# Kernel tuning notes

Measured on AMD Instinct MI355X. Metric: run time of the kernel, lower is better.

The kernel has to match this reference:

```python
import jax, jax.numpy as jnp
import numpy as np

N_TOKEN = 392
POS_WEIGHT = 1.0
LOSS_WEIGHT = 1.0


def _cam_map(logits, w_proj, xf, shape):
    # logits: (B, K_cls); w_proj: (K_cls, C); xf: (B, C, N)
    B, T, H, W = shape
    top_cls = jnp.argmax(logits, axis=1)                 # sort desc -> [0] == argmax
    w_top = w_proj[top_cls]                              # (B, C) gather top-class weight row
    row = jnp.einsum('bc,bcn->bn', w_top, xf)            # (B, N) per-sample CAM scores
    mn = row.min(axis=1, keepdims=True)
    mx = row.max(axis=1, keepdims=True)
    rown = (row - mn) / (mx - mn)                        # min-max normalize
    vals, idxs = jax.lax.top_k(rown, N_TOKEN)            # (B, 392)
    hw = H * W
    ti = idxs // hw
    hi = (idxs % hw) // W
    wi = idxs % W
    bi = jnp.broadcast_to(jnp.arange(B)[:, None], idxs.shape)
    cam = jnp.zeros((B, T, H, W), rown.dtype).at[bi, ti, hi, wi].set(vals)
    return cam


def _forward(x, pred_v_logits, pred_n_logits, w_proj_v, w_proj_n,
             conv_w, conv_b, score_w, score_b):
    B, C, T, H, W = x.shape
    xf = x.reshape(B, C, T * H * W)
    cam_v = _cam_map(pred_v_logits, w_proj_v, xf, (B, T, H, W))
    cam_n = _cam_map(pred_n_logits, w_proj_n, xf, (B, T, H, W))
    cam_gt = jnp.maximum(cam_v, cam_n)                   # torch.where(v > n, v, n)
    cam_gt = jax.lax.stop_gradient(cam_gt)               # original builds it from numpy + .detach()

    dn = ('NCDHW', 'OIDHW', 'NCDHW')
    h1 = jax.nn.relu(
        jax.lax.conv_general_dilated(x, conv_w, (1, 1, 1),
                                     [(0, 0), (1, 1), (1, 1)],
                                     dimension_numbers=dn)
        + conv_b[None, :, None, None, None])
    logits = (jax.lax.conv_general_dilated(h1, score_w, (1, 1, 1),
                                           [(0, 0), (0, 0), (0, 0)],
                                           dimension_numbers=dn)
              + score_b[None, :, None, None, None])      # (B,1,T,H,W)

    xcam = logits[:, 0].reshape(B * T, H * W)
    y = cam_gt.reshape(B * T, H * W)
    # BCEWithLogitsLoss(pos_weight) mean
    bce = -(POS_WEIGHT * y * jax.nn.log_sigmoid(xcam)
            + (1.0 - y) * jax.nn.log_sigmoid(-xcam))
    return LOSS_WEIGHT * bce.mean()


def setup_inputs() -> dict:
    key = jax.random.key(0)
    ks = jax.random.split(key, 8)
    B, C, T, H, W = 64, 256, 32, 7, 7
    Kv, Kn, D = 97, 300, 512
    x = jax.random.normal(ks[0], (B, C, T, H, W), jnp.float32)
    pred_v_logits = jax.random.normal(ks[1], (B, Kv), jnp.float32)
    pred_n_logits = jax.random.normal(ks[2], (B, Kn), jnp.float32)
    w_proj_v = jax.random.normal(ks[3], (Kv, C), jnp.float32) / np.sqrt(C)
    w_proj_n = jax.random.normal(ks[4], (Kn, C), jnp.float32) / np.sqrt(C)
    conv_w = jax.random.normal(ks[5], (D, C, 1, 3, 3), jnp.float32) / np.sqrt(C * 9)
    conv_b = jnp.zeros((D,), jnp.float32)
    score_w = jax.random.normal(ks[6], (1, D, 1, 1, 1), jnp.float32) / np.sqrt(D)
    score_b = jnp.zeros((1,), jnp.float32)
    return {"x": x, "pred_v_logits": pred_v_logits, "pred_n_logits": pred_n_logits,
            "w_proj_v": w_proj_v, "w_proj_n": w_proj_n,
            "conv_w": conv_w, "conv_b": conv_b,
            "score_w": score_w, "score_b": score_b}


def reference(x, pred_v_logits, pred_n_logits, w_proj_v, w_proj_n,
              conv_w, conv_b, score_w, score_b):
    return _forward(x, pred_v_logits, pred_n_logits, w_proj_v, w_proj_n,
                    conv_w, conv_b, score_w, score_b)
```

## Files before the change

kernel.cpp:

```cpp
#include <hip/hip_runtime.h>
#include <hip/hip_bf16.h>
#include <math.h>

#define BB 64
#define CC 256
#define TT 32
#define HH 7
#define WW 7
#define HW 49
#define NN 1568
#define KV 97
#define KN 300
#define DD 512
#define NTOK 392
#define TOTAL (BB*TT*HW)
#define BCAP 256
#define XP_P 257

typedef float f32x4 __attribute__((ext_vector_type(4)));
typedef short bf16x8 __attribute__((ext_vector_type(8)));

#define GLDS(g, l) __builtin_amdgcn_global_load_lds(                          \
    (const __attribute__((address_space(1))) void*)(g),                       \
    (__attribute__((address_space(3))) void*)(l), 16, 0, 0)

__global__ __launch_bounds__(256) void k_xp(
        const float* __restrict__ x, __hip_bfloat16* __restrict__ xp,
        const float* __restrict__ pv, const float* __restrict__ pn,
        const float* __restrict__ wpv, const float* __restrict__ wpn,
        const float* __restrict__ cw, __hip_bfloat16* __restrict__ wb,
        float* __restrict__ rowv, float* __restrict__ rown_,
        int* __restrict__ counter) {
    __shared__ float xs2[HW * XP_P + 7];
    __shared__ float wvs[CC], wns[CC];
    __shared__ float psum[4 * HW];
    __shared__ int cls_sh[2];
    int bt = blockIdx.x;
    int tid = threadIdx.x;
    int b = bt >> 5, t = bt & 31;
    int lane = tid & 63;
    if (bt == 0 && tid == 0) *counter = 0;

    {
        int base = bt * 576;
        #pragma unroll
        for (int r = 0; r < 3; ++r) {
            int o = base + r * 256 + tid;
            if (o < base + 576) {
                int kk = o / (DD * CC);
                int rem = o - kk * (DD * CC);
                int d = rem >> 8, c = rem & 255;
                wb[o] = __float2bfloat16(cw[(d * CC + c) * 9 + kk]);
            }
        }
    }

    if (tid < 128) {
        int head = tid >> 6;
        const float* r = head ? (pn + b * KN) : (pv + b * KV);
        int K = head ? KN : KV;
        float best = -1e30f; int bi = 0x7fffffff;
        for (int k = lane; k < K; k += 64) {
            float v = r[k];
            if (v > best || (v == best && k < bi)) { best = v; bi = k; }
        }
        #pragma unroll
        for (int off = 32; off >= 1; off >>= 1) {
            float ov = __shfl_xor(best, off);
            int oi = __shfl_xor(bi, off);
            if (ov > best || (ov == best && oi < bi)) { best = ov; bi = oi; }
        }
        if (lane == 0) cls_sh[head] = bi;
    }

    const float* xb = x + ((size_t)b * CC * TT + t) * HW;
    for (int i = tid; i < CC * HW; i += 256) {
        int c = i / HW, q = i - (i / HW) * HW;
        xs2[q * XP_P + c] = xb[(size_t)c * (TT * HW) + q];
    }
    __syncthreads();
    wvs[tid] = wpv[cls_sh[0] * CC + tid];
    wns[tid] = wpn[cls_sh[1] * CC + tid];
    __syncthreads();

    __hip_bfloat16* xpb = xp + (size_t)bt * 81 * CC;
    for (int u = tid; u < 81 * 32; u += 256) {
        int p = u >> 5, c0 = (u & 31) * 8;
        int hh = p / 9, ww = p - (p / 9) * 9;
        bool inb = (hh >= 1 && hh <= 7 && ww >= 1 && ww <= 7);
        const float* row = xs2 + ((hh - 1) * 7 + (ww - 1)) * XP_P + c0;
        bf16x8 pack;
        #pragma unroll
        for (int j = 0; j < 8; ++j) {
            float v = inb ? row[j] : 0.f;
            __hip_bfloat16 bv = __float2bfloat16(v);
            pack[j] = *reinterpret_cast<short*>(&bv);
        }
        *reinterpret_cast<bf16x8*>(xpb + p * 256 + c0) = pack;
    }

    if (tid < 4 * HW) {
        int sel = tid / HW;
        int q = tid - sel * HW;
        const float* w = (sel < 2) ? wvs : wns;
        int cb2 = (sel & 1) * 128;
        const float* row = xs2 + q * XP_P + cb2;
        float s = 0.f;
        #pragma unroll 4
        for (int c = 0; c < 128; ++c) s = fmaf(w[cb2 + c], row[c], s);
        psum[tid] = s;
    }
    __syncthreads();
    if (tid < 2 * HW) {
        int head = tid >= HW;
        int q = head ? tid - HW : tid;
        float s = head ? (psum[2 * HW + q] + psum[3 * HW + q])
                       : (psum[q] + psum[HW + q]);
        (head ? rown_ : rowv)[bt * HW + q] = s;
    }
}

__device__ __forceinline__ int binof(float v) {
    int i = (int)(v * 1024.f);
    return i < 0 ? 0 : (i > 1023 ? 1023 : i);
}

__device__ void cam_block(int b, int tid, char* smem,
                          const float* __restrict__ rowv,
                          const float* __restrict__ rown_,
                          float* __restrict__ cam) {
    float* rv = (float*)smem;
    float* rn = (float*)(smem + 6272);
    int* h = (int*)(smem + 12544);
    int* tsum = (int*)(smem + 16640);
    float* lval_v = (float*)(smem + 17664);
    int* lidx_v = (int*)(smem + 18688);
    float* lval_n = (float*)(smem + 19712);
    int* lidx_n = (int*)(smem + 20736);
    float* wred = (float*)(smem + 21760);
    int* sc = (int*)(smem + 21824);

    for (int n = tid; n < NN; n += 256) { rv[n] = rowv[b * NN + n]; rn[n] = rown_[b * NN + n]; }
    __syncthreads();
    float mnv = 1e30f, mxv = -1e30f, mnn = 1e30f, mxn = -1e30f;
    for (int n = tid; n < NN; n += 256) {
        float v = rv[n]; mnv = fminf(mnv, v); mxv = fmaxf(mxv, v);
        float u = rn[n]; mnn = fminf(mnn, u); mxn = fmaxf(mxn, u);
    }
    #pragma unroll
    for (int off = 32; off >= 1; off >>= 1) {
        mnv = fminf(mnv, __shfl_xor(mnv, off));
        mxv = fmaxf(mxv, __shfl_xor(mxv, off));
        mnn = fminf(mnn, __shfl_xor(mnn, off));
        mxn = fmaxf(mxn, __shfl_xor(mxn, off));
    }
    if ((tid & 63) == 0) {
        int wid = tid >> 6;
        wred[wid * 4 + 0] = mnv; wred[wid * 4 + 1] = mxv;
        wred[wid * 4 + 2] = mnn; wred[wid * 4 + 3] = mxn;
    }
    if (tid == 0) { sc[0] = 0; sc[1] = 0; }
    __syncthreads();
    mnv = fminf(fminf(wred[0], wred[4]), fminf(wred[8], wred[12]));
    mxv = fmaxf(fmaxf(wred[1], wred[5]), fmaxf(wred[9], wred[13]));
    mnn = fminf(fminf(wred[2], wred[6]), fminf(wred[10], wred[14]));
    mxn = fmaxf(fmaxf(wred[3], wred[7]), fmaxf(wred[11], wred[15]));
    float iv = 1.f / (mxv - mnv), inn = 1.f / (mxn - mnn);

    for (int n = tid; n < NN; n += 256) {
        rv[n] = (rv[n] - mnv) * iv;
        rn[n] = (rn[n] - mnn) * inn;
    }
    for (int i = tid; i < 1024; i += 256) h[i] = 0;
    __syncthreads();
    for (int n = tid; n < NN; n += 256) {
        atomicAdd(&h[binof(rv[n])], 1);
        atomicAdd(&h[binof(rn[n])], 1 << 16);
    }
    __syncthreads();

    int h0 = h[4 * tid], h1 = h[4 * tid + 1], h2 = h[4 * tid + 2], h3 = h[4 * tid + 3];
    tsum[tid] = h0 + h1 + h2 + h3;
    __syncthreads();
    for (int off = 1; off < 256; off <<= 1) {
        int add = (tid + off < 256) ? tsum[tid + off] : 0;
        __syncthreads();
        tsum[tid] += add;
        __syncthreads();
    }
    {
        int scur = tsum[tid];
        int hk[4] = {h0, h1, h2, h3};
        #pragma unroll
        for (int k = 0; k < 4; ++k) {
            int snext = scur - hk[k];
            int scv = scur & 0xffff, ncv = snext & 0xffff;
            int sh = scur >> 16, nh = snext >> 16;
            if (scv >= NTOK && ncv < NTOK) { sc[2] = 4 * tid + k; sc[3] = ncv; }
            if (sh >= NTOK && nh < NTOK) { sc[4] = 4 * tid + k; sc[5] = nh; }
            scur = snext;
        }
    }
    __syncthreads();
    int bsv = sc[2], abv = sc[3], bsn = sc[4], abn = sc[5];

    for (int n = tid; n < NN; n += 256) {
        float v = rv[n]; int bv = binof(v);
        if (bv < bsv) rv[n] = 0.f;
        else if (bv == bsv) {
            int s = atomicAdd(&sc[0], 1);
            if (s < BCAP) { lval_v[s] = v; lidx_v[s] = n; }
        }
        float u = rn[n]; int bu = binof(u);
        if (bu < bsn) rn[n] = 0.f;
        else if (bu == bsn) {
            int s = atomicAdd(&sc[1], 1);
            if (s < BCAP) { lval_n[s] = u; lidx_n[s] = n; }
        }
    }
    __syncthreads();
    int Lv = sc[0] < BCAP ? sc[0] : BCAP;
    int Ln = sc[1] < BCAP ? sc[1] : BCAP;
    for (int i = tid; i < Lv; i += 256) {
        float vi = lval_v[i]; int ni = lidx_v[i]; int r = 0;
        for (int j = 0; j < Lv; ++j) {
            float vj = lval_v[j]; int nj = lidx_v[j];
            r += (vj > vi || (vj == vi && nj < ni)) ? 1 : 0;
        }
        rv[ni] = (r < NTOK - abv) ? vi : 0.f;
    }
    for (int i = tid; i < Ln; i += 256) {
        float vi = lval_n[i]; int ni = lidx_n[i]; int r = 0;
        for (int j = 0; j < Ln; ++j) {
            float vj = lval_n[j]; int nj = lidx_n[j];
            r += (vj > vi || (vj == vi && nj < ni)) ? 1 : 0;
        }
        rn[ni] = (r < NTOK - abn) ? vi : 0.f;
    }
    __syncthreads();
    for (int n = tid; n < NN; n += 256) cam[b * NN + n] = fmaxf(rv[n], rn[n]);
}

__global__ __launch_bounds__(256, 3) void k_gemm(
        const __hip_bfloat16* __restrict__ xp, const __hip_bfloat16* __restrict__ wb,
        const float* __restrict__ convb, const float* __restrict__ scorew,
        float* __restrict__ pl, const float* __restrict__ rowv,
        const float* __restrict__ rown_, float* __restrict__ cam) {
    __shared__ char smem[32768];
    int tid = threadIdx.x;
    int bid = blockIdx.x;
    if (bid < 64) { cam_block(bid, tid, smem, rowv, rown_, cam); return; }
    char* As = smem;
    char* Bs = smem + 16384;
    int gid = bid - 64;
    int xcd = gid & 7;
    int local = gid >> 3;
    int mtile = xcd * 98 + (local >> 2);
    int nblk = local & 3;
    int m0 = mtile * 128;
    int n0 = nblk * 128;
    int lane = tid & 63, wv = tid >> 6;
    int wm = wv >> 1, wn = wv & 1;
    int ln = lane & 15, qd = lane >> 4;

    int rrow = tid >> 3;
    int segst = ((tid & 7) ^ (rrow & 7)) * 8;
    int bt_[4], hh_[4], ww_[4];
    const __hip_bfloat16* bptr[4];
    #pragma unroll
    for (int j = 0; j < 4; ++j) {
        int m = m0 + j * 32 + rrow;
        int bt = m / HW, q = m - bt * HW;
        bt_[j] = bt; hh_[j] = q / WW; ww_[j] = q - (q / WW) * WW;
        bptr[j] = wb + (size_t)(n0 + j * 32 + rrow) * 256 + segst;
    }

    int swz = ln & 7;
    int offk[2] = {((0 + qd) ^ swz) * 16, ((4 + qd) ^ swz) * 16};

    f32x4 acc[4][4];
    #pragma unroll
    for (int i = 0; i < 4; ++i)
        #pragma unroll
        for (int j = 0; j < 4; ++j) acc[i][j] = (f32x4){0.f, 0.f, 0.f, 0.f};

    for (int kk = 0; kk < 9; ++kk) {
        int kh = kk / 3, kw = kk - (kk / 3) * 3;
        const __hip_bfloat16* aptr[4];
        #pragma unroll
        for (int j = 0; j < 4; ++j)
            aptr[j] = xp + ((size_t)bt_[j] * 81 + (hh_[j] + kh) * 9 + (ww_[j] + kw)) * 256 + segst;
        const size_t boff = (size_t)kk * (DD * 256);
        #pragma unroll
        for (int c0 = 0; c0 < 256; c0 += 64) {
            __syncthreads();
            #pragma unroll
            for (int j = 0; j < 4; ++j) {
                GLDS(aptr[j] + c0, As + j * 4096 + tid * 16);
                GLDS(bptr[j] + boff + c0, Bs + j * 4096 + tid * 16);
            }
            __syncthreads();
            #pragma unroll
            for (int k2 = 0; k2 < 2; ++k2) {
                bf16x8 af[4], bfr[4];
                #pragma unroll
                for (int i = 0; i < 4; ++i)
                    af[i] = *(const bf16x8*)(As + (wm * 64 + i * 16 + ln) * 128 + offk[k2]);
                #pragma unroll
                for (int j = 0; j < 4; ++j)
                    bfr[j] = *(const bf16x8*)(Bs + (wn * 64 + j * 16 + ln) * 128 + offk[k2]);
                #pragma unroll
                for (int i = 0; i < 4; ++i)
                    #pragma unroll
                    for (int j = 0; j < 4; ++j)
                        acc[i][j] = __builtin_amdgcn_mfma_f32_16x16x32_bf16(af[i], bfr[j], acc[i][j], 0, 0, 0);
            }
        }
    }

    float swr[4], cbr[4];
    #pragma unroll
    for (int j = 0; j < 4; ++j) {
        int n = n0 + wn * 64 + j * 16 + ln;
        swr[j] = scorew[n];
        cbr[j] = convb[n];
    }
    float* dst = pl + (size_t)(nblk * 2 + wn) * TOTAL;
    #pragma unroll
    for (int i = 0; i < 4; ++i) {
        #pragma unroll
        for (int r = 0; r < 4; ++r) {
            float v = 0.f;
            #pragma unroll
            for (int j = 0; j < 4; ++j) {
                float h1 = acc[i][j][r] + cbr[j];
                h1 = h1 > 0.f ? h1 : 0.f;
                v = fmaf(swr[j], h1, v);
            }
            v += __shfl_xor(v, 1);
            v += __shfl_xor(v, 2);
            v += __shfl_xor(v, 4);
            v += __shfl_xor(v, 8);
            if (ln == 0)
                dst[m0 + wm * 64 + i * 16 + qd * 4 + r] = v;
        }
    }
}

__global__ __launch_bounds__(256) void k_bce(
        const float* __restrict__ pl, const float* __restrict__ cam,
        const float* __restrict__ sb, float* __restrict__ part,
        int* __restrict__ counter, float* __restrict__ out) {
    __shared__ float sbuf[256];
    __shared__ int isLast;
    int tid = threadIdx.x;
    int m = blockIdx.x * 256 + tid;
    float l = sb[0];
    #pragma unroll
    for (int s = 0; s < 8; ++s) l += pl[(size_t)s * TOTAL + m];
    float y = cam[m];
    float v = fmaxf(l, 0.f) - l * y + log1pf(expf(-fabsf(l)));
    sbuf[tid] = v; __syncthreads();
    for (int k = 128; k > 0; k >>= 1) {
        if (tid < k) sbuf[tid] += sbuf[tid + k];
        __syncthreads();
    }
    if (tid == 0) {
        part[blockIdx.x] = sbuf[0];
        __threadfence();
        int d = atomicAdd(counter, 1);
        isLast = (d == 391);
    }
    __syncthreads();
    if (isLast) {
        float s = 0.f;
        for (int i = tid; i < 392; i += 256) s += part[i];
        sbuf[tid] = s; __syncthreads();
        for (int k = 128; k > 0; k >>= 1) {
            if (tid < k) sbuf[tid] += sbuf[tid + k];
            __syncthreads();
        }
        if (tid == 0) out[0] = sbuf[0] * (1.0f / (float)TOTAL);
    }
}

extern "C" void kernel_launch(void* const* d_in, const int* in_sizes, int n_in,
                              void* d_out, int out_size, void* d_ws, size_t ws_size,
                              hipStream_t stream) {
    const float* x   = (const float*)d_in[0];
    const float* pv  = (const float*)d_in[1];
    const float* pn  = (const float*)d_in[2];
    const float* wpv = (const float*)d_in[3];
    const float* wpn = (const float*)d_in[4];
    const float* cw  = (const float*)d_in[5];
    const float* cb  = (const float*)d_in[6];
    const float* sw  = (const float*)d_in[7];
    const float* sb  = (const float*)d_in[8];

    char* w8 = (char*)d_ws;
    __hip_bfloat16* xp  = (__hip_bfloat16*)w8;
    __hip_bfloat16* wb  = (__hip_bfloat16*)(w8 + 84934656);
    float* pl      = (float*)(w8 + 87293952);
    float* rowv    = (float*)(w8 + 90505216);
    float* rown_   = (float*)(w8 + 90906624);
    float* cam     = (float*)(w8 + 91308032);
    float* part    = (float*)(w8 + 91709440);
    int*   counter = (int*)(w8 + 91711008);

    k_xp<<<2048, 256, 0, stream>>>(x, xp, pv, pn, wpv, wpn, cw, wb,
                                   rowv, rown_, counter);
    k_gemm<<<64 + 3136, 256, 0, stream>>>(xp, wb, cb, sw, pl, rowv, rown_, cam);
    k_bce<<<392, 256, 0, stream>>>(pl, cam, sb, part, counter, (float*)d_out);
}
```

Before: 431.8 us.

## Retile transpose kernel and move CAM projection into cam blocks of gemm

The pre-pass kernel now handles a 32-channel by 8-frame tile per block, reading x with coalesced float4 loads and writing the padded bf16 layout through a smaller padded LDS tile. The per-sample CAM projections (argmax, weight gather, channel dot product) move out of it into the 64 cam blocks of the gemm kernel, which read x directly. This removes the rowv/rown intermediates and the strided per-(b,t) gather of the old transpose. The trade-off is that each cam block now streams 1.6 MB of x serially while it runs beside the gemm blocks, which could lengthen the critical path.

```diff
diff --git a/kernel.cpp b/kernel.cpp
--- a/kernel.cpp
+++ b/kernel.cpp
@@ -15,7 +15,6 @@
 #define NTOK 392
 #define TOTAL (BB*TT*HW)
 #define BCAP 256
-#define XP_P 257
 
 typedef float f32x4 __attribute__((ext_vector_type(4)));
 typedef short bf16x8 __attribute__((ext_vector_type(8)));
@@ -24,25 +23,17 @@
     (const __attribute__((address_space(1))) void*)(g),                       \
     (__attribute__((address_space(3))) void*)(l), 16, 0, 0)
 
-__global__ __launch_bounds__(256) void k_xp(
+__global__ __launch_bounds__(256) void k_tr(
         const float* __restrict__ x, __hip_bfloat16* __restrict__ xp,
-        const float* __restrict__ pv, const float* __restrict__ pn,
-        const float* __restrict__ wpv, const float* __restrict__ wpn,
         const float* __restrict__ cw, __hip_bfloat16* __restrict__ wb,
-        float* __restrict__ rowv, float* __restrict__ rown_,
         int* __restrict__ counter) {
-    __shared__ float xs2[HW * XP_P + 7];
-    __shared__ float wvs[CC], wns[CC];
-    __shared__ float psum[4 * HW];
-    __shared__ int cls_sh[2];
-    int bt = blockIdx.x;
+    __shared__ float xs[392 * 33];
+    int bid = blockIdx.x;
     int tid = threadIdx.x;
-    int b = bt >> 5, t = bt & 31;
-    int lane = tid & 63;
-    if (bt == 0 && tid == 0) *counter = 0;
+    if (bid == 0 && tid == 0) *counter = 0;
 
     {
-        int base = bt * 576;
+        int base = bid * 576;
         #pragma unroll
         for (int r = 0; r < 3; ++r) {
             int o = base + r * 256 + tid;
@@ -55,40 +46,49 @@
         }
     }
 
-    if (tid < 128) {
-        int head = tid >> 6;
-        const float* r = head ? (pn + b * KN) : (pv + b * KV);
-        int K = head ? KN : KV;
-        float best = -1e30f; int bi = 0x7fffffff;
-        for (int k = lane; k < K; k += 64) {
-            float v = r[k];
-            if (v > best || (v == best && k < bi)) { best = v; bi = k; }
-        }
-        #pragma unroll
-        for (int off = 32; off >= 1; off >>= 1) {
-            float ov = __shfl_xor(best, off);
-            int oi = __shfl_xor(bi, off);
-            if (ov > best || (ov == best && oi < bi)) { best = ov; bi = oi; }
-        }
-        if (lane == 0) cls_sh[head] = bi;
-    }
-
-    const float* xb = x + ((size_t)b * CC * TT + t) * HW;
-    for (int i = tid; i < CC * HW; i += 256) {
-        int c = i / HW, q = i - (i / HW) * HW;
-        xs2[q * XP_P + c] = xb[(size_t)c * (TT * HW) + q];
-    }
-    __syncthreads();
-    wvs[tid] = wpv[cls_sh[0] * CC + tid];
-    wns[tid] = wpn[cls_sh[1] * CC + tid];
-    __syncthreads();
-
-    __hip_bfloat16* xpb = xp + (size_t)bt * 81 * CC;
-    for (int u = tid; u < 81 * 32; u += 256) {
-        int p = u >> 5, c0 = (u & 31) * 8;
+    int b  = bid >> 5;
+    int cc = (bid >> 2) & 7;
+    int tc = bid & 3;
+    int c0 = cc << 5;
+    int t0 = tc << 3;
+
+    const float* xbase = x + ((size_t)((b * CC + c0) * TT + t0)) * HW;
+    const float4* xb4 = (const float4*)xbase;
+    for (int base = 0; base < 3072; base += 1024) {
+        float4 v[4]; int li[4];
+        #pragma unroll
+        for (int j = 0; j < 4; ++j) {
+            int idx = base + j * 256 + tid;
+            v[j] = xb4[idx];
+            int ch = idx / 98, o4 = idx - ch * 98;
+            li[j] = (o4 * 4) * 33 + ch;
+        }
+        #pragma unroll
+        for (int j = 0; j < 4; ++j) {
+            xs[li[j]     ] = v[j].x;
+            xs[li[j] + 33] = v[j].y;
+            xs[li[j] + 66] = v[j].z;
+            xs[li[j] + 99] = v[j].w;
+        }
+    }
+    {
+        int idx = 3072 + tid;
+        if (idx < 3136) {
+            float4 v = xb4[idx];
+            int ch = idx / 98, o4 = idx - ch * 98;
+            int li = (o4 * 4) * 33 + ch;
+            xs[li] = v.x; xs[li + 33] = v.y; xs[li + 66] = v.z; xs[li + 99] = v.w;
+        }
+    }
+    __syncthreads();
+
+    __hip_bfloat16* xpb = xp + ((size_t)(b * TT + t0) * 81) * 256 + c0;
+    for (int u = tid; u < 2592; u += 256) {
+        int pos = u >> 2, cq = u & 3;
+        int tt = pos / 81, p = pos - tt * 81;
         int hh = p / 9, ww = p - (p / 9) * 9;
         bool inb = (hh >= 1 && hh <= 7 && ww >= 1 && ww <= 7);
-        const float* row = xs2 + ((hh - 1) * 7 + (ww - 1)) * XP_P + c0;
+        const float* row = xs + (tt * 49 + (hh - 1) * 7 + (ww - 1)) * 33 + cq * 8;
         bf16x8 pack;
         #pragma unroll
         for (int j = 0; j < 8; ++j) {
@@ -96,27 +96,7 @@
             __hip_bfloat16 bv = __float2bfloat16(v);
             pack[j] = *reinterpret_cast<short*>(&bv);
         }
-        *reinterpret_cast<bf16x8*>(xpb + p * 256 + c0) = pack;
-    }
-
-    if (tid < 4 * HW) {
-        int sel = tid / HW;
-        int q = tid - sel * HW;
-        const float* w = (sel < 2) ? wvs : wns;
-        int cb2 = (sel & 1) * 128;
-        const float* row = xs2 + q * XP_P + cb2;
-        float s = 0.f;
-        #pragma unroll 4
-        for (int c = 0; c < 128; ++c) s = fmaf(w[cb2 + c], row[c], s);
-        psum[tid] = s;
-    }
-    __syncthreads();
-    if (tid < 2 * HW) {
-        int head = tid >= HW;
-        int q = head ? tid - HW : tid;
-        float s = head ? (psum[2 * HW + q] + psum[3 * HW + q])
-                       : (psum[q] + psum[HW + q]);
-        (head ? rown_ : rowv)[bt * HW + q] = s;
+        *reinterpret_cast<bf16x8*>(xpb + (size_t)(tt * 81 + p) * 256 + cq * 8) = pack;
     }
 }
 
@@ -126,8 +106,9 @@
 }
 
 __device__ void cam_block(int b, int tid, char* smem,
-                          const float* __restrict__ rowv,
-                          const float* __restrict__ rown_,
+                          const float* __restrict__ x,
+                          const float* __restrict__ pv, const float* __restrict__ pn,
+                          const float* __restrict__ wpv, const float* __restrict__ wpn,
                           float* __restrict__ cam) {
     float* rv = (float*)smem;
     float* rn = (float*)(smem + 6272);
@@ -139,9 +120,65 @@
     int* lidx_n = (int*)(smem + 20736);
     float* wred = (float*)(smem + 21760);
     int* sc = (int*)(smem + 21824);
-
-    for (int n = tid; n < NN; n += 256) { rv[n] = rowv[b * NN + n]; rn[n] = rown_[b * NN + n]; }
-    __syncthreads();
+    float* wvs = (float*)(smem + 21888);
+    float* wns = (float*)(smem + 22912);
+    int* cls2 = (int*)(smem + 23936);
+
+    int lane = tid & 63;
+    if (tid < 128) {
+        int head = tid >> 6;
+        const float* r = head ? (pn + b * KN) : (pv + b * KV);
+        int K = head ? KN : KV;
+        float best = -1e30f; int bi = 0x7fffffff;
+        for (int k = lane; k < K; k += 64) {
+            float v = r[k];
+            if (v > best || (v == best && k < bi)) { best = v; bi = k; }
+        }
+        #pragma unroll
+        for (int off = 32; off >= 1; off >>= 1) {
+            float ov = __shfl_xor(best, off);
+            int oi = __shfl_xor(bi, off);
+            if (ov > best || (ov == best && oi < bi)) { best = ov; bi = oi; }
+        }
+        if (lane == 0) cls2[head] = bi;
+    }
+    __syncthreads();
+    wvs[tid] = wpv[cls2[0] * CC + tid];
+    wns[tid] = wpn[cls2[1] * CC + tid];
+    __syncthreads();
+
+    {
+        const f32x4* xb4 = (const f32x4*)(x + (size_t)b * CC * NN);
+        bool two = tid < (392 - 256);
+        f32x4 av0 = {0.f,0.f,0.f,0.f}, an0 = {0.f,0.f,0.f,0.f};
+        f32x4 av1 = {0.f,0.f,0.f,0.f}, an1 = {0.f,0.f,0.f,0.f};
+        for (int c = 0; c < CC; ++c) {
+            float wv = wvs[c], wn = wns[c];
+            const f32x4* rowc = xb4 + (size_t)c * 392;
+            f32x4 u0 = rowc[tid];
+            #pragma unroll
+            for (int r = 0; r < 4; ++r) {
+                av0[r] = fmaf(wv, u0[r], av0[r]);
+                an0[r] = fmaf(wn, u0[r], an0[r]);
+            }
+            if (two) {
+                f32x4 u1 = rowc[tid + 256];
+                #pragma unroll
+                for (int r = 0; r < 4; ++r) {
+                    av1[r] = fmaf(wv, u1[r], av1[r]);
+                    an1[r] = fmaf(wn, u1[r], an1[r]);
+                }
+            }
+        }
+        *reinterpret_cast<f32x4*>(rv + 4 * tid) = av0;
+        *reinterpret_cast<f32x4*>(rn + 4 * tid) = an0;
+        if (two) {
+            *reinterpret_cast<f32x4*>(rv + 4 * (tid + 256)) = av1;
+            *reinterpret_cast<f32x4*>(rn + 4 * (tid + 256)) = an1;
+        }
+    }
+    __syncthreads();
+
     float mnv = 1e30f, mxv = -1e30f, mnn = 1e30f, mxn = -1e30f;
     for (int n = tid; n < NN; n += 256) {
         float v = rv[n]; mnv = fminf(mnv, v); mxv = fmaxf(mxv, v);
@@ -244,12 +281,15 @@
 __global__ __launch_bounds__(256, 3) void k_gemm(
         const __hip_bfloat16* __restrict__ xp, const __hip_bfloat16* __restrict__ wb,
         const float* __restrict__ convb, const float* __restrict__ scorew,
-        float* __restrict__ pl, const float* __restrict__ rowv,
-        const float* __restrict__ rown_, float* __restrict__ cam) {
+        float* __restrict__ pl,
+        const float* __restrict__ x,
+        const float* __restrict__ pv, const float* __restrict__ pn,
+        const float* __restrict__ wpv, const float* __restrict__ wpn,
+        float* __restrict__ cam) {
     __shared__ char smem[32768];
     int tid = threadIdx.x;
     int bid = blockIdx.x;
-    if (bid < 64) { cam_block(bid, tid, smem, rowv, rown_, cam); return; }
+    if (bid < 64) { cam_block(bid, tid, smem, x, pv, pn, wpv, wpn, cam); return; }
     char* As = smem;
     char* Bs = smem + 16384;
     int gid = bid - 64;
@@ -401,14 +441,12 @@
     __hip_bfloat16* xp  = (__hip_bfloat16*)w8;
     __hip_bfloat16* wb  = (__hip_bfloat16*)(w8 + 84934656);
     float* pl      = (float*)(w8 + 87293952);
-    float* rowv    = (float*)(w8 + 90505216);
-    float* rown_   = (float*)(w8 + 90906624);
-    float* cam     = (float*)(w8 + 91308032);
-    float* part    = (float*)(w8 + 91709440);
-    int*   counter = (int*)(w8 + 91711008);
-
-    k_xp<<<2048, 256, 0, stream>>>(x, xp, pv, pn, wpv, wpn, cw, wb,
-                                   rowv, rown_, counter);
-    k_gemm<<<64 + 3136, 256, 0, stream>>>(xp, wb, cb, sw, pl, rowv, rown_, cam);
+    float* cam     = (float*)(w8 + 90505216);
+    float* part    = (float*)(w8 + 90906624);
+    int*   counter = (int*)(w8 + 90908192);
+
+    k_tr<<<2048, 256, 0, stream>>>(x, xp, cw, wb, counter);
+    k_gemm<<<64 + 3136, 256, 0, stream>>>(xp, wb, cb, sw, pl,
+                                          x, pv, pn, wpv, wpn, cam);
     k_bce<<<392, 256, 0, stream>>>(pl, cam, sb, part, counter, (float*)d_out);
 }
```

New measurement: 411.6 us. -4.7%, faster.
